# Optimization experiments

Hardware: AMD Instinct MI355X
Metric: run time of the kernel (lower is better)

## Reference

```python
import jax, jax.numpy as jnp
import numpy as np

N, E = 50000, 800000
F_IN, H, C = 128, 4, 32
NEG_SLOPE = 0.2

def setup_inputs() -> dict:
    key = jax.random.key(0)
    k1, k2, k3, k4, k5, k6 = jax.random.split(key, 6)
    x = jax.random.normal(k1, (N, F_IN), dtype=jnp.float32)
    edge_index = jax.random.randint(k2, (2, E), 0, N, dtype=jnp.int64)
    # GATConv params: lin weight [F_IN, H*C], att_src/att_dst [H, C], bias [H*C]
    W = jax.random.normal(k3, (F_IN, H * C), dtype=jnp.float32) * (1.0 / np.sqrt(F_IN))
    att_src = jax.random.normal(k4, (H, C), dtype=jnp.float32) * (1.0 / np.sqrt(C))
    att_dst = jax.random.normal(k5, (H, C), dtype=jnp.float32) * (1.0 / np.sqrt(C))
    bias = jax.random.normal(k6, (H * C,), dtype=jnp.float32) * 0.01
    return {"x": x, "edge_index": edge_index, "W": W, "att_src": att_src, "att_dst": att_dst, "bias": bias}

def reference(x, edge_index, W, att_src, att_dst, bias):
    # Linear transform: [N, H, C]
    h = (x @ W).reshape(N, H, C)
    # Per-node attention logits: [N, H]
    a_src = jnp.einsum('nhc,hc->nh', h, att_src)
    a_dst = jnp.einsum('nhc,hc->nh', h, att_dst)
    # PyG GATConv adds self-loops by default
    loop = jnp.arange(N, dtype=edge_index.dtype)
    src = jnp.concatenate([edge_index[0], loop])  # message source j
    dst = jnp.concatenate([edge_index[1], loop])  # message target i
    # Edge logits + LeakyReLU: [E+N, H]
    e = jax.nn.leaky_relu(a_src[src] + a_dst[dst], NEG_SLOPE)
    # Segment softmax over incoming edges per target node
    m = jax.ops.segment_max(e, dst, num_segments=N)  # [N, H]
    e_exp = jnp.exp(e - m[dst])
    denom = jax.ops.segment_sum(e_exp, dst, num_segments=N)  # [N, H]
    att = e_exp / denom[dst]  # [E+N, H]
    # Scatter-add weighted messages: [N, H, C]
    out = jax.ops.segment_sum(h[src] * att[:, :, None], dst, num_segments=N)
    return out.reshape(N, H * C) + bias
```

## Files before the change

kernel.cpp:

```cpp
#include <hip/hip_runtime.h>
#include <cstdint>

#define NNODES 50000
#define NEDGES 800000
#define NEG 0.2f
#define NBKT 196
#define BCAP 5120

typedef __attribute__((ext_vector_type(8))) short short8;
typedef __attribute__((ext_vector_type(4))) float f32x4;

#define AS_STRIDE 136
#define CS_STRIDE 132

__device__ __forceinline__ float leaky(float v) { return v > 0.f ? v : NEG * v; }

__device__ __forceinline__ unsigned short f2bf(float f) {
    unsigned int u = __float_as_uint(f);
    u += 0x7fff + ((u >> 16) & 1);
    return (unsigned short)(u >> 16);
}

__device__ __forceinline__ int block_excl_scan(int v, int t) {
    __shared__ int wsum[4];
    const int lane = t & 63, wv = t >> 6;
    int x = v;
    #pragma unroll
    for (int m = 1; m < 64; m <<= 1) {
        int u = __shfl_up(x, m);
        if (lane >= m) x += u;
    }
    if (lane == 63) wsum[wv] = x;
    __syncthreads();
    if (t == 0) {
        int run = 0;
        #pragma unroll
        for (int i = 0; i < 4; ++i) { int tmp = wsum[i]; wsum[i] = run; run += tmp; }
    }
    __syncthreads();
    return x - v + wsum[wv];
}

__global__ __launch_bounds__(256) void gemm_k(const float* __restrict__ x,
                                              const float* __restrict__ W,
                                              unsigned short* __restrict__ hb,
                                              const float* __restrict__ att_src,
                                              const float* __restrict__ att_dst,
                                              float* __restrict__ a_src,
                                              float* __restrict__ a_dst) {
    __shared__ __align__(16) char smem[52224];
    unsigned short* As = (unsigned short*)smem;
    unsigned short* Bs = (unsigned short*)(smem + 17408);
    float*          Cs = (float*)smem;

    const int tid = threadIdx.x;
    const int rbase = blockIdx.x * 64;

    #pragma unroll
    for (int i = 0; i < 8; ++i) {
        int f = tid + i * 256;
        int r = f >> 5, c4 = (f & 31) * 4;
        float4 xv = make_float4(0.f, 0.f, 0.f, 0.f);
        if (rbase + r < NNODES) xv = ((const float4*)x)[(size_t)(rbase + r) * 32 + (f & 31)];
        unsigned int p0 = ((unsigned int)f2bf(xv.y) << 16) | f2bf(xv.x);
        unsigned int p1 = ((unsigned int)f2bf(xv.w) << 16) | f2bf(xv.z);
        *(uint2*)(As + r * AS_STRIDE + c4) = make_uint2(p0, p1);
    }
    #pragma unroll
    for (int i = 0; i < 64; ++i) {
        int f = tid + i * 256;
        int k = f >> 7, n = f & 127;
        Bs[n * AS_STRIDE + k] = f2bf(W[f]);
    }
    __syncthreads();

    const int lane = tid & 63, w = tid >> 6;
    const int quad = lane >> 4, m16 = lane & 15;

    short8 af[4];
    #pragma unroll
    for (int s = 0; s < 4; ++s)
        af[s] = *(const short8*)(As + (w * 16 + m16) * AS_STRIDE + s * 32 + quad * 8);

    f32x4 acc[8];
    #pragma unroll
    for (int t = 0; t < 8; ++t) acc[t] = (f32x4){0.f, 0.f, 0.f, 0.f};

    #pragma unroll
    for (int t = 0; t < 8; ++t) {
        #pragma unroll
        for (int s = 0; s < 4; ++s) {
            short8 bf = *(const short8*)(Bs + (t * 16 + m16) * AS_STRIDE + s * 32 + quad * 8);
            acc[t] = __builtin_amdgcn_mfma_f32_16x16x32_bf16(af[s], bf, acc[t], 0, 0, 0);
        }
    }
    __syncthreads();

    #pragma unroll
    for (int t = 0; t < 8; ++t)
        #pragma unroll
        for (int r = 0; r < 4; ++r)
            Cs[(w * 16 + quad * 4 + r) * CS_STRIDE + t * 16 + m16] = acc[t][r];
    __syncthreads();

    const int cp = lane;
    float2 as_v = ((const float2*)att_src)[cp];
    float2 ad_v = ((const float2*)att_dst)[cp];
    #pragma unroll
    for (int r = 0; r < 16; ++r) {
        int row = w * 16 + r;
        int row_g = rbase + row;
        float2 cv = *(const float2*)(Cs + row * CS_STRIDE + 2 * cp);
        ushort2 hs;
        hs.x = f2bf(cv.x); hs.y = f2bf(cv.y);
        if (row_g < NNODES) ((ushort2*)(hb + (size_t)row_g * 128))[cp] = hs;
        float ps = cv.x * as_v.x + cv.y * as_v.y;
        float pd = cv.x * ad_v.x + cv.y * ad_v.y;
        #pragma unroll
        for (int m = 8; m >= 1; m >>= 1) {
            ps += __shfl_xor(ps, m, 16);
            pd += __shfl_xor(pd, m, 16);
        }
        if (row_g < NNODES && (cp & 15) == 0) {
            a_src[row_g * 4 + (cp >> 4)] = ps;
            a_dst[row_g * 4 + (cp >> 4)] = pd;
        }
    }
}

__global__ __launch_bounds__(256) void bin_k(const int* __restrict__ ei,
                                             int* __restrict__ bcnt,
                                             unsigned int* __restrict__ bktdata) {
    __shared__ int lhist[NBKT];
    __shared__ int lofs[NBKT];
    __shared__ int lcur[NBKT];
    __shared__ int gbase[NBKT];
    __shared__ unsigned int staged[4096];
    const int b = blockIdx.x, t = threadIdx.x;
    for (int i = t; i < NBKT; i += 256) lhist[i] = 0;
    __syncthreads();
    unsigned int pk[16];
    int bk[16];
    const int e0 = b * 4096;
    #pragma unroll
    for (int i = 0; i < 16; ++i) {
        int e = e0 + i * 256 + t;
        if (e < NEDGES) {
            int s = ei[e], d = ei[NEDGES + e];
            bk[i] = d >> 8;
            pk[i] = ((unsigned)bk[i] << 24) | ((unsigned)(d & 255) << 16) | (unsigned)s;
            atomicAdd(&lhist[bk[i]], 1);
        } else bk[i] = -1;
    }
    __syncthreads();
    int v = (t < NBKT) ? lhist[t] : 0;
    int excl = block_excl_scan(v, t);
    if (t < NBKT) { lofs[t] = excl; lcur[t] = excl; }
    __syncthreads();
    if (t < NBKT) gbase[t] = (v > 0) ? atomicAdd(&bcnt[t], v) : 0;
    #pragma unroll
    for (int i = 0; i < 16; ++i) {
        if (bk[i] >= 0) {
            int pos = atomicAdd(&lcur[bk[i]], 1);
            staged[pos] = pk[i];
        }
    }
    __syncthreads();
    const int total = lofs[NBKT - 1] + lhist[NBKT - 1];
    for (int i = t; i < total; i += 256) {
        unsigned int ent = staged[i];
        int bb = ent >> 24;
        int pos = gbase[bb] + (i - lofs[bb]);
        bktdata[(size_t)bb * BCAP + pos] = ent & 0x00FFFFFFu;
    }
}

__global__ __launch_bounds__(256) void bscan_k(const int* __restrict__ bcnt,
                                               int* __restrict__ bktoff) {
    const int t = threadIdx.x;
    int v = (t < NBKT) ? bcnt[t] : 0;
    int excl = block_excl_scan(v, t);
    if (t < NBKT) bktoff[t] = excl;
}

__global__ __launch_bounds__(256) void sort_k(const int* __restrict__ bcnt,
                                              const int* __restrict__ bktoff,
                                              const unsigned int* __restrict__ bktdata,
                                              int* __restrict__ off,
                                              int* __restrict__ csr) {
    __shared__ unsigned int staged[BCAP];
    __shared__ int sorted[BCAP];
    __shared__ int lcnt[256];
    __shared__ int lcur[256];
    const int b = blockIdx.x, t = threadIdx.x;
    const int cnt = bcnt[b], base = bktoff[b];
    lcnt[t] = 0;
    for (int i = t; i < cnt; i += 256) staged[i] = bktdata[(size_t)b * BCAP + i];
    __syncthreads();
    for (int i = t; i < cnt; i += 256) atomicAdd(&lcnt[staged[i] >> 16], 1);
    __syncthreads();
    int v = lcnt[t];
    int excl = block_excl_scan(v, t);
    lcur[t] = excl;
    const int node = b * 256 + t;
    if (node <= NNODES) off[node] = base + excl;
    __syncthreads();
    for (int i = t; i < cnt; i += 256) {
        unsigned int ent = staged[i];
        int pos = atomicAdd(&lcur[ent >> 16], 1);
        sorted[pos] = (int)(ent & 0xFFFFu);
    }
    __syncthreads();
    for (int i = t; i < cnt; i += 256) csr[base + i] = sorted[i];
}

__global__ __launch_bounds__(256) void gather_k(const int* __restrict__ off,
                                                const int* __restrict__ csr,
                                                const unsigned short* __restrict__ hb,
                                                const float* __restrict__ a_src,
                                                const float* __restrict__ a_dst,
                                                const float* __restrict__ bias,
                                                float* __restrict__ out) {
    const int wid = threadIdx.x >> 6, lane = threadIdx.x & 63;
    const int n = blockIdx.x * 4 + wid;
    if (n >= NNODES) return;
    const int head = lane >> 4;
    const int sub = lane & 15;

    const float a_d = a_dst[n * 4 + head];
    const float w_self = __expf(leaky(a_src[n * 4 + head] + a_d));
    unsigned int hv0 = ((const unsigned int*)(hb + (size_t)n * 128))[lane];
    float hnx = __uint_as_float(hv0 << 16);
    float hny = __uint_as_float(hv0 & 0xffff0000u);
    float accx = w_self * hnx, accy = w_self * hny;
    float denom = w_self;

    const int beg = off[n], end = off[n + 1];
    for (int base = beg; base < end; base += 16) {
        int m = end - base; if (m > 16) m = 16;
        int s = 0;
        float w = 0.f;
        if (sub < m) {
            s = csr[base + sub];
            w = __expf(leaky(a_src[s * 4 + head] + a_d));
        }
        if (m == 16) {
            #pragma unroll
            for (int j = 0; j < 16; ++j) {
                int   sj = __shfl(s, j);
                float wj = __shfl(w, (head << 4) | j);
                unsigned int hv = ((const unsigned int*)(hb + (size_t)sj * 128))[lane];
                float hx = __uint_as_float(hv << 16);
                float hy = __uint_as_float(hv & 0xffff0000u);
                denom += wj;
                accx += wj * hx; accy += wj * hy;
            }
        } else {
            for (int j = 0; j < m; ++j) {
                int   sj = __shfl(s, j);
                float wj = __shfl(w, (head << 4) | j);
                unsigned int hv = ((const unsigned int*)(hb + (size_t)sj * 128))[lane];
                float hx = __uint_as_float(hv << 16);
                float hy = __uint_as_float(hv & 0xffff0000u);
                denom += wj;
                accx += wj * hx; accy += wj * hy;
            }
        }
    }
    const float inv = __frcp_rn(denom);
    float2 bv = ((const float2*)bias)[lane];
    ((float2*)(out + (size_t)n * 128))[lane] =
        make_float2(accx * inv + bv.x, accy * inv + bv.y);
}

extern "C" void kernel_launch(void* const* d_in, const int* in_sizes, int n_in,
                              void* d_out, int out_size, void* d_ws, size_t ws_size,
                              hipStream_t stream) {
    const float* x     = (const float*)d_in[0];
    const int*   ei    = (const int*)d_in[1];
    const float* W     = (const float*)d_in[2];
    const float* att_s = (const float*)d_in[3];
    const float* att_d = (const float*)d_in[4];
    const float* bias  = (const float*)d_in[5];
    float*       out   = (float*)d_out;
    char*        ws    = (char*)d_ws;

    unsigned short* hb = (unsigned short*)(ws);
    float* a_src  = (float*)(ws + 12800000);
    float* a_dst  = (float*)(ws + 13600000);
    int*   off    = (int*)  (ws + 14400000);
    int*   csr    = (int*)  (ws + 14600768);
    unsigned int* bktdata = (unsigned int*)(ws + 17800768);
    int*   bcnt   = (int*)  (ws + 21814848);
    int*   bktoff = (int*)  (ws + 21815680);

    hipMemsetAsync(bcnt, 0, NBKT * sizeof(int), stream);
    gemm_k  <<<782,   256, 0, stream>>>(x, W, hb, att_s, att_d, a_src, a_dst);
    bin_k   <<<196,   256, 0, stream>>>(ei, bcnt, bktdata);
    bscan_k <<<1,     256, 0, stream>>>(bcnt, bktoff);
    sort_k  <<<196,   256, 0, stream>>>(bcnt, bktoff, bktdata, off, csr);
    gather_k<<<12500, 256, 0, stream>>>(off, csr, hb, a_src, a_dst, bias, out);
}
```

Baseline: 169.2 us.

## Gather four neighbor rows per iteration with 16-byte loads in gather kernel

Restructures the per-node aggregation so each wavefront splits into four 16-lane groups. Each group loads a different neighbor's full bf16 feature row with uint4 (16-byte) loads and keeps 8 accumulators per lane. Partial sums are combined across groups with xor shuffles at the end, and the softmax denominator is reduced with a segmented shuffle. The aim is fewer, wider memory requests and more independent loads in flight per iteration. The cost is extra registers, cross-lane reductions, and predicated loads for partial chunks.

```diff
diff --git a/kernel.cpp b/kernel.cpp
--- a/kernel.cpp
+++ b/kernel.cpp
@@ -225,15 +225,28 @@
     const int n = blockIdx.x * 4 + wid;
     if (n >= NNODES) return;
     const int head = lane >> 4;
-    const int sub = lane & 15;
+    const int sub  = lane & 15;
+    const int g = head, q = sub;
+    const int head_c = q >> 2;
 
     const float a_d = a_dst[n * 4 + head];
-    const float w_self = __expf(leaky(a_src[n * 4 + head] + a_d));
-    unsigned int hv0 = ((const unsigned int*)(hb + (size_t)n * 128))[lane];
-    float hnx = __uint_as_float(hv0 << 16);
-    float hny = __uint_as_float(hv0 & 0xffff0000u);
-    float accx = w_self * hnx, accy = w_self * hny;
-    float denom = w_self;
+    float acc[8];
+    #pragma unroll
+    for (int k = 0; k < 8; ++k) acc[k] = 0.f;
+
+    if (g == 0) {
+        float wsc = __expf(leaky(a_src[n * 4 + head_c] + a_dst[n * 4 + head_c]));
+        uint4 hv = ((const uint4*)(hb + (size_t)n * 128))[q];
+        acc[0] = wsc * __uint_as_float(hv.x << 16);
+        acc[1] = wsc * __uint_as_float(hv.x & 0xffff0000u);
+        acc[2] = wsc * __uint_as_float(hv.y << 16);
+        acc[3] = wsc * __uint_as_float(hv.y & 0xffff0000u);
+        acc[4] = wsc * __uint_as_float(hv.z << 16);
+        acc[5] = wsc * __uint_as_float(hv.z & 0xffff0000u);
+        acc[6] = wsc * __uint_as_float(hv.w << 16);
+        acc[7] = wsc * __uint_as_float(hv.w & 0xffff0000u);
+    }
+    float denom = (sub == 0) ? __expf(leaky(a_src[n * 4 + head] + a_d)) : 0.f;
 
     const int beg = off[n], end = off[n + 1];
     for (int base = beg; base < end; base += 16) {
@@ -244,33 +257,42 @@
             s = csr[base + sub];
             w = __expf(leaky(a_src[s * 4 + head] + a_d));
         }
-        if (m == 16) {
-            #pragma unroll
-            for (int j = 0; j < 16; ++j) {
-                int   sj = __shfl(s, j);
-                float wj = __shfl(w, (head << 4) | j);
-                unsigned int hv = ((const unsigned int*)(hb + (size_t)sj * 128))[lane];
-                float hx = __uint_as_float(hv << 16);
-                float hy = __uint_as_float(hv & 0xffff0000u);
-                denom += wj;
-                accx += wj * hx; accy += wj * hy;
+        denom += w;
+        #pragma unroll
+        for (int jj = 0; jj < 4; ++jj) {
+            int j = jj * 4 + g;
+            int   sj = __shfl(s, j);
+            float wj = __shfl(w, (head_c << 4) | j);
+            if (j < m) {
+                uint4 hv = ((const uint4*)(hb + (size_t)sj * 128))[q];
+                acc[0] += wj * __uint_as_float(hv.x << 16);
+                acc[1] += wj * __uint_as_float(hv.x & 0xffff0000u);
+                acc[2] += wj * __uint_as_float(hv.y << 16);
+                acc[3] += wj * __uint_as_float(hv.y & 0xffff0000u);
+                acc[4] += wj * __uint_as_float(hv.z << 16);
+                acc[5] += wj * __uint_as_float(hv.z & 0xffff0000u);
+                acc[6] += wj * __uint_as_float(hv.w << 16);
+                acc[7] += wj * __uint_as_float(hv.w & 0xffff0000u);
             }
-        } else {
-            for (int j = 0; j < m; ++j) {
-                int   sj = __shfl(s, j);
-                float wj = __shfl(w, (head << 4) | j);
-                unsigned int hv = ((const unsigned int*)(hb + (size_t)sj * 128))[lane];
-                float hx = __uint_as_float(hv << 16);
-                float hy = __uint_as_float(hv & 0xffff0000u);
-                denom += wj;
-                accx += wj * hx; accy += wj * hy;
-            }
-        }
-    }
-    const float inv = __frcp_rn(denom);
-    float2 bv = ((const float2*)bias)[lane];
-    ((float2*)(out + (size_t)n * 128))[lane] =
-        make_float2(accx * inv + bv.x, accy * inv + bv.y);
+        }
+    }
+    #pragma unroll
+    for (int mm = 8; mm >= 1; mm >>= 1) denom += __shfl_xor(denom, mm, 16);
+    const float inv = __frcp_rn(__shfl(denom, head_c << 4));
+    #pragma unroll
+    for (int k = 0; k < 8; ++k) {
+        acc[k] += __shfl_xor(acc[k], 16);
+        acc[k] += __shfl_xor(acc[k], 32);
+    }
+    if (g == 0) {
+        float4 b0 = ((const float4*)bias)[2 * q];
+        float4 b1 = ((const float4*)bias)[2 * q + 1];
+        float4* orow = (float4*)(out + (size_t)n * 128);
+        orow[2 * q]     = make_float4(acc[0] * inv + b0.x, acc[1] * inv + b0.y,
+                                      acc[2] * inv + b0.z, acc[3] * inv + b0.w);
+        orow[2 * q + 1] = make_float4(acc[4] * inv + b1.x, acc[5] * inv + b1.y,
+                                      acc[6] * inv + b1.z, acc[7] * inv + b1.w);
+    }
 }
 
 extern "C" void kernel_launch(void* const* d_in, const int* in_sizes, int n_in,
```

Result: no change. 170.1 us (+0.6%).
